# Kernel optimization log

Measured on AMD Instinct MI355X. Metric: run time of the kernel, lower is better.

The kernel has to match this reference:

```python
import jax, jax.numpy as jnp
import numpy as np

N = 50000      # nodes
E = 200000     # edges (before self-loops)
HID = 64       # hidden_channels
HEADS = 8
VOCAB = 100    # node-type vocabulary for the embedding
NEG_SLOPE = 0.2
EPS = 1e-16


def _gatv2(x, src, dst, Wl, bl, Wr, br, att, bias, heads, out_ch):
    """GATv2Conv (PyG defaults: share_weights=False, concat=True, neg_slope=0.2).
    x: [N, F_in]; src/dst: [E_tot] (self-loops already appended).
    Returns [N, heads*out_ch]."""
    n = x.shape[0]
    xl = (x @ Wl + bl).reshape(n, heads, out_ch)   # source transform
    xr = (x @ Wr + br).reshape(n, heads, out_ch)   # target transform
    m = xl[src] + xr[dst]                          # [E, H, C]
    e = jnp.einsum('ehc,hc->eh', jax.nn.leaky_relu(m, NEG_SLOPE), att)  # [E, H]
    # segment softmax over incoming edges of each destination node
    e_max = jax.ops.segment_max(e, dst, num_segments=n)
    e_exp = jnp.exp(e - e_max[dst])
    denom = jax.ops.segment_sum(e_exp, dst, num_segments=n)
    alpha = e_exp / (denom[dst] + EPS)             # [E, H]
    out = jax.ops.segment_sum(alpha[:, :, None] * xl[src], dst, num_segments=n)
    return out.reshape(n, heads * out_ch) + bias


def setup_inputs() -> dict:
    key = jax.random.key(0)
    ks = jax.random.split(key, 16)
    s = 0.1
    return {
        'x': jax.random.randint(ks[0], (N,), 0, VOCAB),
        'edge_index': jax.random.randint(ks[1], (2, E), 0, N),
        'emb': jax.random.normal(ks[2], (VOCAB, HID), dtype=jnp.float32) * s,
        'Wl1': jax.random.normal(ks[3], (HID, HEADS * HID), dtype=jnp.float32) * s,
        'bl1': jnp.zeros((HEADS * HID,), jnp.float32),
        'Wr1': jax.random.normal(ks[4], (HID, HEADS * HID), dtype=jnp.float32) * s,
        'br1': jnp.zeros((HEADS * HID,), jnp.float32),
        'att1': jax.random.normal(ks[5], (HEADS, HID), dtype=jnp.float32) * s,
        'bias1': jnp.zeros((HEADS * HID,), jnp.float32),
        'Wl2': jax.random.normal(ks[6], (HEADS * HID, 2), dtype=jnp.float32) * s,
        'bl2': jnp.zeros((2,), jnp.float32),
        'Wr2': jax.random.normal(ks[7], (HEADS * HID, 2), dtype=jnp.float32) * s,
        'br2': jnp.zeros((2,), jnp.float32),
        'att2': jax.random.normal(ks[8], (1, 2), dtype=jnp.float32) * s,
        'bias2': jnp.zeros((2,), jnp.float32),
    }


def reference(x, edge_index, emb, Wl1, bl1, Wr1, br1, att1, bias1,
              Wl2, bl2, Wr2, br2, att2, bias2):
    # PyG GATv2Conv adds self-loops by default
    loops = jnp.arange(N, dtype=edge_index.dtype)
    src = jnp.concatenate([edge_index[0], loops])
    dst = jnp.concatenate([edge_index[1], loops])

    h = emb[x]                                       # embedding lookup [N, HID]
    # dropout layers are identity in eval mode
    h = _gatv2(h, src, dst, Wl1, bl1, Wr1, br1, att1, bias1, HEADS, HID)
    h = jax.nn.elu(h)
    out = _gatv2(h, src, dst, Wl2, bl2, Wr2, br2, att2, bias2, 1, 2)
    return out                                       # [N, 2]
```

## Files before the change

kernel.cpp:

```cpp
#include <hip/hip_runtime.h>
#include <math.h>

#define NEG_SLOPE 0.2f
#define EPSV 1e-16f
#define CAP 32

__global__ __launch_bounds__(256) void kA_tables_fill(
    const float* __restrict__ emb, const float* __restrict__ Wl1,
    const float* __restrict__ bl1, const float* __restrict__ Wr1,
    const float* __restrict__ br1,
    const int* __restrict__ srcE, const int* __restrict__ dstE,
    const int* __restrict__ x,
    float* __restrict__ table_l, float* __restrict__ table_r,
    int* __restrict__ cnt, int* __restrict__ adj,
    int nb_tab, int nb_E, int E, int N, int VOCAB, int tshift)
{
    int b = blockIdx.x;
    if (b < nb_tab) {
        int idx = b * 256 + threadIdx.x;
        if (idx < VOCAB * 512) {
            int t = idx >> 9, o = idx & 511;
            float sl = bl1[o], sr = br1[o];
            const float* e = emb + t * 64;
            #pragma unroll 8
            for (int k = 0; k < 64; ++k) {
                float ev = e[k];
                sl = fmaf(ev, Wl1[k * 512 + o], sl);
                sr = fmaf(ev, Wr1[k * 512 + o], sr);
            }
            table_l[idx] = sl;
            table_r[idx] = sr;
        }
    } else if (b < nb_tab + nb_E) {
        int e = (b - nb_tab) * 256 + threadIdx.x;
        if (e < E) {
            int d = dstE[e];
            int sv = srcE[e];
            int pos = atomicAdd(&cnt[d], 1);
            if (pos < CAP) adj[d * CAP + pos] = (sv << tshift) | x[sv];
        }
    } else {
        int d = (b - nb_tab - nb_E) * 256 + threadIdx.x;
        if (d < N) {
            int pos = atomicAdd(&cnt[d], 1);
            if (pos < CAP) adj[d * CAP + pos] = (d << tshift) | x[d];
        }
    }
}

__global__ __launch_bounds__(256) void kB_epair(
    const float* __restrict__ table_l, const float* __restrict__ table_r,
    const float* __restrict__ att1, float* __restrict__ exp_pair, int VOCAB)
{
    int idx = blockIdx.x * 256 + threadIdx.x;
    if (idx >= VOCAB * VOCAB * 8) return;
    int h = idx & 7;
    int p = idx >> 3;
    int ts = p % VOCAB;
    int td = p / VOCAB;
    const float4* tl = (const float4*)(table_l + ts * 512 + h * 64);
    const float4* tr = (const float4*)(table_r + td * 512 + h * 64);
    const float4* a  = (const float4*)(att1 + h * 64);
    float s = 0.f;
    #pragma unroll
    for (int c4 = 0; c4 < 16; ++c4) {
        float4 l = tl[c4], r = tr[c4], av = a[c4];
        float m0 = l.x + r.x; m0 = m0 > 0.f ? m0 : NEG_SLOPE * m0; s = fmaf(m0, av.x, s);
        float m1 = l.y + r.y; m1 = m1 > 0.f ? m1 : NEG_SLOPE * m1; s = fmaf(m1, av.y, s);
        float m2 = l.z + r.z; m2 = m2 > 0.f ? m2 : NEG_SLOPE * m2; s = fmaf(m2, av.z, s);
        float m3 = l.w + r.w; m3 = m3 > 0.f ? m3 : NEG_SLOPE * m3; s = fmaf(m3, av.w, s);
    }
    exp_pair[idx] = __expf(s);
}

__global__ __launch_bounds__(256) void k4_node_agg(
    const int* __restrict__ x, const int* __restrict__ cnt,
    const int* __restrict__ adj,
    const float* __restrict__ table_l, const float* __restrict__ exp_pair,
    const float* __restrict__ bias1,
    const float* __restrict__ Wl2, const float* __restrict__ bl2,
    const float* __restrict__ Wr2, const float* __restrict__ br2,
    float2* __restrict__ xl2, float2* __restrict__ xr2,
    int N, int VOCAB, int tmask)
{
    int wid = blockIdx.x * 4 + (threadIdx.x >> 6);
    if (wid >= N) return;
    int lane = threadIdx.x & 63;
    int h8 = lane & 7;
    int e8 = lane >> 3;
    int hc = lane >> 3;
    int d = wid;
    int start = d * CAP;

    int aw = adj[start + e8];
    int td = x[d];
    int deg = min(cnt[d], CAP);
    int ts = aw & tmask;
    const float* ep = exp_pair + (size_t)td * VOCAB * 8;
    float w = ep[ts * 8 + h8];
    if (e8 >= deg) w = 0.f;
    float sw = w;

    float acc[8] = {0.f, 0.f, 0.f, 0.f, 0.f, 0.f, 0.f, 0.f};
    int deg8 = min(deg, 8);

    #pragma unroll
    for (int e = 0; e < 8; ++e) {
        int se = e < deg8 ? e : (deg8 - 1);
        float we = e < deg8 ? __shfl(w, (e << 3) | hc) : 0.f;
        int tse = __shfl(ts, se << 3);
        const float4* row = (const float4*)(table_l + (size_t)tse * 512 + lane * 8);
        float4 r0 = row[0], r1 = row[1];
        acc[0] = fmaf(we, r0.x, acc[0]); acc[1] = fmaf(we, r0.y, acc[1]);
        acc[2] = fmaf(we, r0.z, acc[2]); acc[3] = fmaf(we, r0.w, acc[3]);
        acc[4] = fmaf(we, r1.x, acc[4]); acc[5] = fmaf(we, r1.y, acc[5]);
        acc[6] = fmaf(we, r1.z, acc[6]); acc[7] = fmaf(we, r1.w, acc[7]);
    }
    for (int base = 8; base < deg; base += 8) {
        int eidx = base + e8;
        bool v2 = eidx < deg;
        int aw2 = adj[start + (v2 ? eidx : 0)];
        int ts2 = aw2 & tmask;
        float w2 = v2 ? ep[ts2 * 8 + h8] : 0.f;
        sw += w2;
        int nche = min(deg - base, 8);
        for (int e = 0; e < nche; ++e) {
            float we = __shfl(w2, (e << 3) | hc);
            int tse = __shfl(ts2, e << 3);
            const float4* row = (const float4*)(table_l + (size_t)tse * 512 + lane * 8);
            float4 r0 = row[0], r1 = row[1];
            acc[0] = fmaf(we, r0.x, acc[0]); acc[1] = fmaf(we, r0.y, acc[1]);
            acc[2] = fmaf(we, r0.z, acc[2]); acc[3] = fmaf(we, r0.w, acc[3]);
            acc[4] = fmaf(we, r1.x, acc[4]); acc[5] = fmaf(we, r1.y, acc[5]);
            acc[6] = fmaf(we, r1.z, acc[6]); acc[7] = fmaf(we, r1.w, acc[7]);
        }
    }
    float sden = sw;
    sden += __shfl_xor(sden, 8);
    sden += __shfl_xor(sden, 16);
    sden += __shfl_xor(sden, 32);
    float inv_dn = 1.f / (__shfl(sden, hc) + EPSV);

    const float4* b4 = (const float4*)(bias1 + lane * 8);
    float4 b0 = b4[0], b1 = b4[1];
    float bb[8] = {b0.x, b0.y, b0.z, b0.w, b1.x, b1.y, b1.z, b1.w};
    float h1[8];
    #pragma unroll
    for (int j = 0; j < 8; ++j) {
        float v = fmaf(acc[j], inv_dn, bb[j]);
        h1[j] = v > 0.f ? v : (__expf(v) - 1.f);
    }
    const float4* wl4 = (const float4*)(Wl2 + lane * 16);
    const float4* wr4 = (const float4*)(Wr2 + lane * 16);
    float sl0 = 0.f, sl1 = 0.f, sr0 = 0.f, sr1 = 0.f;
    #pragma unroll
    for (int k = 0; k < 4; ++k) {
        float4 vl = wl4[k], vr = wr4[k];
        float ha = h1[2 * k], hb = h1[2 * k + 1];
        sl0 = fmaf(ha, vl.x, sl0); sl1 = fmaf(ha, vl.y, sl1);
        sl0 = fmaf(hb, vl.z, sl0); sl1 = fmaf(hb, vl.w, sl1);
        sr0 = fmaf(ha, vr.x, sr0); sr1 = fmaf(ha, vr.y, sr1);
        sr0 = fmaf(hb, vr.z, sr0); sr1 = fmaf(hb, vr.w, sr1);
    }
    #pragma unroll
    for (int mm = 1; mm < 64; mm <<= 1) {
        sl0 += __shfl_xor(sl0, mm);
        sl1 += __shfl_xor(sl1, mm);
        sr0 += __shfl_xor(sr0, mm);
        sr1 += __shfl_xor(sr1, mm);
    }
    if (lane == 0) {
        xl2[d] = make_float2(sl0 + bl2[0], sl1 + bl2[1]);
        xr2[d] = make_float2(sr0 + br2[0], sr1 + br2[1]);
    }
}

__global__ __launch_bounds__(256) void k5_layer2(
    const int* __restrict__ cnt, const int* __restrict__ adj,
    const float2* __restrict__ xl2, const float2* __restrict__ xr2,
    const float* __restrict__ att2, const float* __restrict__ bias2,
    float2* __restrict__ out, int N, int tshift)
{
    int wid = blockIdx.x * 4 + (threadIdx.x >> 6);
    int lane = threadIdx.x & 63;
    int g = lane >> 3, j = lane & 7;
    int d = wid * 8 + g;
    int dc = min(d, N - 1);
    int start = dc * CAP;
    float a0 = att2[0], a1 = att2[1];

    int aw = adj[start + j];
    int deg = min(cnt[dc], CAP);
    float2 xr = xr2[dc];
    int src = min(aw >> tshift, N - 1);
    float2 xl = xl2[src];
    float m0 = xl.x + xr.x; m0 = m0 > 0.f ? m0 : NEG_SLOPE * m0;
    float m1 = xl.y + xr.y; m1 = m1 > 0.f ? m1 : NEG_SLOPE * m1;
    float ev = fmaf(a0, m0, a1 * m1);
    float w = (j < deg) ? __expf(ev) : 0.f;
    float s = w, o0 = w * xl.x, o1 = w * xl.y;

    for (int e = j + 8; e < deg; e += 8) {
        int src2 = min(adj[start + e] >> tshift, N - 1);
        float2 x2 = xl2[src2];
        float n0 = x2.x + xr.x; n0 = n0 > 0.f ? n0 : NEG_SLOPE * n0;
        float n1 = x2.y + xr.y; n1 = n1 > 0.f ? n1 : NEG_SLOPE * n1;
        float e2 = fmaf(a0, n0, a1 * n1);
        float w2 = __expf(e2);
        s += w2;
        o0 = fmaf(w2, x2.x, o0);
        o1 = fmaf(w2, x2.y, o1);
    }
    #pragma unroll
    for (int off = 1; off < 8; off <<= 1) {
        s  += __shfl_xor(s, off);
        o0 += __shfl_xor(o0, off);
        o1 += __shfl_xor(o1, off);
    }
    if (d < N && j == 0) {
        float inv = 1.f / (s + EPSV);
        out[d] = make_float2(fmaf(o0, inv, bias2[0]), fmaf(o1, inv, bias2[1]));
    }
}

extern "C" void kernel_launch(void* const* d_in, const int* in_sizes, int n_in,
                              void* d_out, int out_size, void* d_ws, size_t ws_size,
                              hipStream_t stream) {
    (void)n_in; (void)out_size; (void)ws_size;
    const int*   x     = (const int*)d_in[0];
    const int*   ei    = (const int*)d_in[1];
    const float* emb   = (const float*)d_in[2];
    const float* Wl1   = (const float*)d_in[3];
    const float* bl1   = (const float*)d_in[4];
    const float* Wr1   = (const float*)d_in[5];
    const float* br1   = (const float*)d_in[6];
    const float* att1  = (const float*)d_in[7];
    const float* bias1 = (const float*)d_in[8];
    const float* Wl2   = (const float*)d_in[9];
    const float* bl2   = (const float*)d_in[10];
    const float* Wr2   = (const float*)d_in[11];
    const float* br2   = (const float*)d_in[12];
    const float* att2  = (const float*)d_in[13];
    const float* bias2 = (const float*)d_in[14];
    float* out = (float*)d_out;

    int N = in_sizes[0];
    int E = in_sizes[1] / 2;
    int VOCAB = in_sizes[2] / 64;
    const int* srcE = ei;
    const int* dstE = ei + E;

    int tshift = 1;
    while ((1 << tshift) < VOCAB) ++tshift;
    int tmask = (1 << tshift) - 1;

    float* table_l  = (float*)d_ws;
    float* table_r  = table_l + (size_t)VOCAB * 512;
    float* exp_pair = table_r + (size_t)VOCAB * 512;
    int*   cnt      = (int*)(exp_pair + (size_t)VOCAB * VOCAB * 8);
    int*   adj      = cnt + N + (N & 1);
    float* xl2      = (float*)(adj + (size_t)N * CAP);
    float* xr2      = xl2 + 2 * (size_t)N;

    hipMemsetAsync(cnt, 0, sizeof(int) * (size_t)N, stream);

    int nb_tab = (VOCAB * 512 + 255) / 256;
    int nb_E = (E + 255) / 256;
    int nb_N = (N + 255) / 256;

    kA_tables_fill<<<nb_tab + nb_E + nb_N, 256, 0, stream>>>(
        emb, Wl1, bl1, Wr1, br1, srcE, dstE, x,
        table_l, table_r, cnt, adj, nb_tab, nb_E, E, N, VOCAB, tshift);

    int nb_ep = (VOCAB * VOCAB * 8 + 255) / 256;
    kB_epair<<<nb_ep, 256, 0, stream>>>(table_l, table_r, att1, exp_pair, VOCAB);

    k4_node_agg<<<(N + 3) / 4, 256, 0, stream>>>(
        x, cnt, adj, table_l, exp_pair, bias1, Wl2, bl2, Wr2, br2,
        (float2*)xl2, (float2*)xr2, N, VOCAB, tmask);

    k5_layer2<<<(N + 31) / 32, 256, 0, stream>>>(
        cnt, adj, (const float2*)xl2, (const float2*)xr2,
        att2, bias2, (float2*)out, N, tshift);
}
```

Baseline: 171.1 us.

## Reserve self-loop slot in adjacency and batch-load edge rows per lane in layer-1 aggregation

Self-loops now always occupy slot 0 of each adjacency row and no longer take an atomic, so the count only tracks real edges. The layer-1 aggregation reads the first eight adjacency entries as two int4 loads. Every lane then issues all eight weight and table-row loads before accumulating, replacing the per-edge shuffle pattern with independent loads in flight. The tail is processed in groups of four. Each lane computes the denominator directly, removing the cross-lane reduction, at the cost of redundant weight loads and higher register pressure.

```diff
diff --git a/kernel.cpp b/kernel.cpp
--- a/kernel.cpp
+++ b/kernel.cpp
@@ -36,15 +36,12 @@
         if (e < E) {
             int d = dstE[e];
             int sv = srcE[e];
-            int pos = atomicAdd(&cnt[d], 1);
+            int pos = 1 + atomicAdd(&cnt[d], 1);
             if (pos < CAP) adj[d * CAP + pos] = (sv << tshift) | x[sv];
         }
     } else {
         int d = (b - nb_tab - nb_E) * 256 + threadIdx.x;
-        if (d < N) {
-            int pos = atomicAdd(&cnt[d], 1);
-            if (pos < CAP) adj[d * CAP + pos] = (d << tshift) | x[d];
-        }
+        if (d < N) adj[d * CAP] = (d << tshift) | x[d];
     }
 }
 
@@ -83,63 +80,78 @@
     float2* __restrict__ xl2, float2* __restrict__ xr2,
     int N, int VOCAB, int tmask)
 {
-    int wid = blockIdx.x * 4 + (threadIdx.x >> 6);
+    int wid = __builtin_amdgcn_readfirstlane(blockIdx.x * 4 + (threadIdx.x >> 6));
     if (wid >= N) return;
     int lane = threadIdx.x & 63;
-    int h8 = lane & 7;
-    int e8 = lane >> 3;
     int hc = lane >> 3;
-    int d = wid;
-    int start = d * CAP;
-
-    int aw = adj[start + e8];
-    int td = x[d];
-    int deg = min(cnt[d], CAP);
-    int ts = aw & tmask;
-    const float* ep = exp_pair + (size_t)td * VOCAB * 8;
-    float w = ep[ts * 8 + h8];
-    if (e8 >= deg) w = 0.f;
-    float sw = w;
-
+
+    const int* arow = adj + wid * CAP;
+    int4 A0 = ((const int4*)arow)[0];
+    int4 A1 = ((const int4*)arow)[1];
+    int deg = min(cnt[wid], CAP - 1) + 1;
+    int td = x[wid];
+    const float* ep = exp_pair + (size_t)td * (VOCAB * 8);
+    int tclamp = VOCAB - 1;
+
+    int ts[8];
+    ts[0] = min(A0.x & tmask, tclamp); ts[1] = min(A0.y & tmask, tclamp);
+    ts[2] = min(A0.z & tmask, tclamp); ts[3] = min(A0.w & tmask, tclamp);
+    ts[4] = min(A1.x & tmask, tclamp); ts[5] = min(A1.y & tmask, tclamp);
+    ts[6] = min(A1.z & tmask, tclamp); ts[7] = min(A1.w & tmask, tclamp);
+    int ts0 = ts[0];
+    #pragma unroll
+    for (int e = 1; e < 8; ++e) if (e >= deg) ts[e] = ts0;
+
+    float we[8];
+    #pragma unroll
+    for (int e = 0; e < 8; ++e) we[e] = ep[ts[e] * 8 + hc];
+    float4 r0[8], r1[8];
+    #pragma unroll
+    for (int e = 0; e < 8; ++e) {
+        const float4* rp = (const float4*)(table_l + (size_t)ts[e] * 512 + lane * 8);
+        r0[e] = rp[0];
+        r1[e] = rp[1];
+    }
+    float sw = 0.f;
     float acc[8] = {0.f, 0.f, 0.f, 0.f, 0.f, 0.f, 0.f, 0.f};
-    int deg8 = min(deg, 8);
-
     #pragma unroll
     for (int e = 0; e < 8; ++e) {
-        int se = e < deg8 ? e : (deg8 - 1);
-        float we = e < deg8 ? __shfl(w, (e << 3) | hc) : 0.f;
-        int tse = __shfl(ts, se << 3);
-        const float4* row = (const float4*)(table_l + (size_t)tse * 512 + lane * 8);
-        float4 r0 = row[0], r1 = row[1];
-        acc[0] = fmaf(we, r0.x, acc[0]); acc[1] = fmaf(we, r0.y, acc[1]);
-        acc[2] = fmaf(we, r0.z, acc[2]); acc[3] = fmaf(we, r0.w, acc[3]);
-        acc[4] = fmaf(we, r1.x, acc[4]); acc[5] = fmaf(we, r1.y, acc[5]);
-        acc[6] = fmaf(we, r1.z, acc[6]); acc[7] = fmaf(we, r1.w, acc[7]);
-    }
-    for (int base = 8; base < deg; base += 8) {
-        int eidx = base + e8;
-        bool v2 = eidx < deg;
-        int aw2 = adj[start + (v2 ? eidx : 0)];
-        int ts2 = aw2 & tmask;
-        float w2 = v2 ? ep[ts2 * 8 + h8] : 0.f;
-        sw += w2;
-        int nche = min(deg - base, 8);
-        for (int e = 0; e < nche; ++e) {
-            float we = __shfl(w2, (e << 3) | hc);
-            int tse = __shfl(ts2, e << 3);
-            const float4* row = (const float4*)(table_l + (size_t)tse * 512 + lane * 8);
-            float4 r0 = row[0], r1 = row[1];
-            acc[0] = fmaf(we, r0.x, acc[0]); acc[1] = fmaf(we, r0.y, acc[1]);
-            acc[2] = fmaf(we, r0.z, acc[2]); acc[3] = fmaf(we, r0.w, acc[3]);
-            acc[4] = fmaf(we, r1.x, acc[4]); acc[5] = fmaf(we, r1.y, acc[5]);
-            acc[6] = fmaf(we, r1.z, acc[6]); acc[7] = fmaf(we, r1.w, acc[7]);
-        }
-    }
-    float sden = sw;
-    sden += __shfl_xor(sden, 8);
-    sden += __shfl_xor(sden, 16);
-    sden += __shfl_xor(sden, 32);
-    float inv_dn = 1.f / (__shfl(sden, hc) + EPSV);
+        float w = (e < deg) ? we[e] : 0.f;
+        sw += w;
+        acc[0] = fmaf(w, r0[e].x, acc[0]); acc[1] = fmaf(w, r0[e].y, acc[1]);
+        acc[2] = fmaf(w, r0[e].z, acc[2]); acc[3] = fmaf(w, r0[e].w, acc[3]);
+        acc[4] = fmaf(w, r1[e].x, acc[4]); acc[5] = fmaf(w, r1[e].y, acc[5]);
+        acc[6] = fmaf(w, r1[e].z, acc[6]); acc[7] = fmaf(w, r1[e].w, acc[7]);
+    }
+    for (int base = 8; base < deg; base += 4) {
+        int t4[4];
+        #pragma unroll
+        for (int u = 0; u < 4; ++u) {
+            int e = base + u;
+            int aw = (e < deg) ? arow[e] : arow[0];
+            t4[u] = min(aw & tmask, tclamp);
+        }
+        float w4[4];
+        #pragma unroll
+        for (int u = 0; u < 4; ++u) w4[u] = ep[t4[u] * 8 + hc];
+        float4 s0[4], s1[4];
+        #pragma unroll
+        for (int u = 0; u < 4; ++u) {
+            const float4* rp = (const float4*)(table_l + (size_t)t4[u] * 512 + lane * 8);
+            s0[u] = rp[0];
+            s1[u] = rp[1];
+        }
+        #pragma unroll
+        for (int u = 0; u < 4; ++u) {
+            float w = (base + u < deg) ? w4[u] : 0.f;
+            sw += w;
+            acc[0] = fmaf(w, s0[u].x, acc[0]); acc[1] = fmaf(w, s0[u].y, acc[1]);
+            acc[2] = fmaf(w, s0[u].z, acc[2]); acc[3] = fmaf(w, s0[u].w, acc[3]);
+            acc[4] = fmaf(w, s1[u].x, acc[4]); acc[5] = fmaf(w, s1[u].y, acc[5]);
+            acc[6] = fmaf(w, s1[u].z, acc[6]); acc[7] = fmaf(w, s1[u].w, acc[7]);
+        }
+    }
+    float inv_dn = 1.f / (sw + EPSV);
 
     const float4* b4 = (const float4*)(bias1 + lane * 8);
     float4 b0 = b4[0], b1 = b4[1];
@@ -170,8 +182,8 @@
         sr1 += __shfl_xor(sr1, mm);
     }
     if (lane == 0) {
-        xl2[d] = make_float2(sl0 + bl2[0], sl1 + bl2[1]);
-        xr2[d] = make_float2(sr0 + br2[0], sr1 + br2[1]);
+        xl2[wid] = make_float2(sl0 + bl2[0], sl1 + bl2[1]);
+        xr2[wid] = make_float2(sr0 + br2[0], sr1 + br2[1]);
     }
 }
 
@@ -190,7 +202,7 @@
     float a0 = att2[0], a1 = att2[1];
 
     int aw = adj[start + j];
-    int deg = min(cnt[dc], CAP);
+    int deg = min(cnt[dc], CAP - 1) + 1;
     float2 xr = xr2[dc];
     int src = min(aw >> tshift, N - 1);
     float2 xl = xl2[src];
@@ -258,7 +270,7 @@
     float* table_r  = table_l + (size_t)VOCAB * 512;
     float* exp_pair = table_r + (size_t)VOCAB * 512;
     int*   cnt      = (int*)(exp_pair + (size_t)VOCAB * VOCAB * 8);
-    int*   adj      = cnt + N + (N & 1);
+    int*   adj      = cnt + ((N + 3) & ~3);
     float* xl2      = (float*)(adj + (size_t)N * CAP);
     float* xr2      = xl2 + 2 * (size_t)N;
 
```

New measurement: 172.1 us. Within noise of the previous version (+0.6%).
